# Performance work log

Measured on AMD Instinct MI355X. Metric: run time of the kernel, lower is better.

Reference implementation:

```python
import jax, jax.numpy as jnp
import numpy as np

B, FC, FRAMES, C = 8, 256, 512, 256


def conv1d(x, w, stride=1, pad=(0, 0), dil=1):
    # x: [N, Cin, L], w: [Cout, Cin, K]
    return jax.lax.conv_general_dilated(
        x, w, window_strides=(stride,), padding=[pad],
        rhs_dilation=(dil,), dimension_numbers=('NCH', 'OIH', 'NCH'))


def setup_inputs() -> dict:
    key = jax.random.key(0)
    ks = jax.random.split(key, 8)
    s = 0.05
    x = jax.random.normal(ks[0], (B, FC, FRAMES), dtype=jnp.float32)
    enc_w0 = jax.random.normal(ks[1], (128, 1, 7), dtype=jnp.float32) * s
    enc_w123 = jax.random.normal(ks[2], (3, 128, 128, 7), dtype=jnp.float32) * s
    enc_w4567 = jax.random.normal(ks[3], (4, 128, 128, 3), dtype=jnp.float32) * s
    enc_w8 = jax.random.normal(ks[4], (C, 128, 1), dtype=jnp.float32) * s
    main_w = jax.random.normal(ks[5], (8, C, C, 2), dtype=jnp.float32) * s
    gate_w = jax.random.normal(ks[6], (8, C, C, 2), dtype=jnp.float32) * s
    judge_w = jax.random.normal(ks[7], (1, C, 1), dtype=jnp.float32) * s
    return {'x': x, 'enc_w0': enc_w0, 'enc_w123': enc_w123,
            'enc_w4567': enc_w4567, 'enc_w8': enc_w8,
            'main_w': main_w, 'gate_w': gate_w, 'judge_w': judge_w}


def reference(x, enc_w0, enc_w123, enc_w4567, enc_w8, main_w, gate_w, judge_w):
    lrelu = lambda h: jax.nn.leaky_relu(h, 0.2)
    b = x.shape[0]
    # [B, FC, FRAMES] -> [B*FRAMES, 1, FC]: encode each frame's feature vector
    h = jnp.transpose(x, (0, 2, 1)).reshape(-1, 1, FC)
    h = lrelu(conv1d(h, enc_w0, stride=2, pad=(3, 3)))
    for i in range(3):
        h = lrelu(conv1d(h, enc_w123[i], stride=2, pad=(3, 3)))
    for i in range(4):
        h = lrelu(conv1d(h, enc_w4567[i], stride=2, pad=(1, 1)))
    h = conv1d(h, enc_w8)                       # [B*FRAMES, C, 1], no activation
    h = jnp.transpose(h.reshape(b, FRAMES, C), (0, 2, 1))  # [B, C, FRAMES]
    # WaveNet stack: causal pad + dilated k=2 convs + tanh*sigmoid gate + residual
    feats = jnp.zeros_like(h)
    for i in range(8):
        p = 2 ** i
        z = jnp.tanh(conv1d(h, main_w[i], pad=(p, 0), dil=p)) * \
            jax.nn.sigmoid(conv1d(h, gate_w[i], pad=(p, 0), dil=p))
        feats = feats + z
        h = z + h                              # channels always match -> residual
    latent = feats
    j = conv1d(latent, judge_w)[:, :, -1:]      # [B, 1, 1]
    return latent[:, :, -1:], j
```

## Files before the change

kernel.cpp:

```cpp
#include <hip/hip_runtime.h>
#include <math.h>

#define FC 256
#define NB 8
#define RS 136

typedef __attribute__((ext_vector_type(8))) _Float16 f16x8;
typedef __attribute__((ext_vector_type(4))) float f32x4;

__device__ __forceinline__ float lrelu(float v) { return fmaxf(v, 0.2f * v); }
__device__ __forceinline__ unsigned short f2h(float f) {
  _Float16 h = (_Float16)f;
  return *(unsigned short*)&h;
}
__device__ __forceinline__ void bar() { asm volatile("s_barrier" ::: "memory"); }
__device__ __forceinline__ void wait_lgkm0() { asm volatile("s_waitcnt lgkmcnt(0)" ::: "memory"); }

#define N1 344064
#define N2 196608
#define N3 32768
#define NTOT 573440
#define NWN 2097152

__global__ void pack_kernel(const float* __restrict__ w123,
                            const float* __restrict__ w4567,
                            const float* __restrict__ w8,
                            const float* __restrict__ mw,
                            const float* __restrict__ gw,
                            unsigned short* __restrict__ wp,
                            unsigned short* __restrict__ wn) {
  int idx = blockIdx.x * 512 + threadIdx.x;
  if (idx < N1) {
    int e = idx & 7, lane = (idx >> 3) & 63, ct = (idx >> 9) & 7, ks = (idx >> 12) & 3, t = idx >> 14;
    int l = t / 7, kw = t % 7;
    int co = ct * 16 + (lane & 15), ci = ks * 32 + (lane >> 4) * 8 + e;
    wp[idx] = f2h(w123[(((l * 128 + co) * 128) + ci) * 7 + kw]);
  } else if (idx < N1 + N2) {
    int k = idx - N1;
    int e = k & 7, lane = (k >> 3) & 63, ct = (k >> 9) & 7, ks = (k >> 12) & 3, t = k >> 14;
    int l = t / 3, kw = t % 3;
    int co = ct * 16 + (lane & 15), ci = ks * 32 + (lane >> 4) * 8 + e;
    wp[idx] = f2h(w4567[(((l * 128 + co) * 128) + ci) * 3 + kw]);
  } else if (idx < NTOT) {
    int k = idx - N1 - N2;
    int e = k & 7, lane = (k >> 3) & 63, ct = (k >> 9) & 15, ks = (k >> 13) & 3;
    int co = ct * 16 + (lane & 15), ci = ks * 32 + (lane >> 4) * 8 + e;
    wp[idx] = f2h(w8[co * 128 + ci]);
  } else if (idx < NTOT + NWN) {
    int k2 = idx - NTOT;
    int li = k2 >> 18, w = k2 & 262143;
    int e = w & 7, lane = (w >> 3) & 63, rt = (w >> 9) & 31, k32 = w >> 14;
    int row = rt * 16 + (lane & 15), k = k32 * 32 + (lane >> 4) * 8 + e;
    int ch = row >> 1, mat = row & 1, kw = k >> 8, ci = k & 255;
    const float* src = mat ? gw : mw;
    wn[k2] = f2h(src[(((size_t)li * 256 + ch) * 256 + ci) * 2 + kw]);
  }
}

template<int KW, int POFF, int PIN, int POUT, int MC, int MN, int OM>
__device__ __forceinline__ void mlayer_d2(const unsigned short* __restrict__ wp,
                                          const unsigned short* __restrict__ sin0,
                                          const unsigned short* __restrict__ sin1,
                                          unsigned short* __restrict__ sout0,
                                          unsigned short* __restrict__ sout1,
                                          unsigned short* __restrict__ gact,
                                          int tid, int frame0) {
  constexpr int HRIN = PIN / 2 + 4;
  constexpr int HROUT = POUT / 2 + 4;
  constexpr int Nt = (POUT + 15) / 16;
  constexpr int MNg = Nt / MN;
  constexpr int MCg = 8 / MNg;
  static_assert(MC * MCg == 8, "cout tiling must cover 128 channels");
  constexpr int NS = KW * 4;
  constexpr int DA = NS < 6 ? NS : 6;
  constexpr int DB = NS < 3 ? NS : 3;

  const int wid = tid >> 6, lane = tid & 63, nl = lane & 15, q = lane >> 4;
  const int q8 = q * 8;
  const int mcg = wid / MNg, mng = wid % MNg;
  const int ct0 = mcg * MC, nt0 = mng * MN;

  const unsigned short* sins[2] = {sin0, sin1};
  unsigned short* souts[2] = {sout0, sout1};

  int jj[MN]; bool val[MN]; int rb[MN][KW]; int rx[MN][KW];
#pragma unroll
  for (int jn = 0; jn < MN; ++jn) {
    int n = (nt0 + jn) * 16 + nl;
    val[jn] = (n < POUT);
    jj[jn] = val[jn] ? n : 0;
#pragma unroll
    for (int kw = 0; kw < KW; ++kw) {
      int P = 2 * jj[jn] + kw - POFF + 4;
      int row = (P & 1) * HRIN + (P >> 1);
      rb[jn][kw] = row * 128;
      rx[jn][kw] = (row & 7) << 3;
    }
  }
  const unsigned short* wl = wp + (size_t)ct0 * 512 + lane * 8;

  f32x4 acc[MC][MN][2];
#pragma unroll
  for (int i = 0; i < MC; ++i)
#pragma unroll
    for (int jn = 0; jn < MN; ++jn)
#pragma unroll
      for (int f = 0; f < 2; ++f) acc[i][jn][f] = (f32x4){0.f, 0.f, 0.f, 0.f};

  f16x8 A[DA][MC], B[DB][MN][2];
#pragma unroll
  for (int s = 0; s < DA; ++s)
#pragma unroll
    for (int i = 0; i < MC; ++i)
      A[s][i] = *(const f16x8*)(wl + (size_t)s * 4096 + i * 512);
#pragma unroll
  for (int s = 0; s < DB; ++s) {
    const int kw = s >> 2, ks = s & 3;
#pragma unroll
    for (int jn = 0; jn < MN; ++jn)
#pragma unroll
      for (int f = 0; f < 2; ++f)
        B[s][jn][f] = *(const f16x8*)(sins[f] + rb[jn][kw] + ((ks * 32 + q8) ^ rx[jn][kw]));
  }
#pragma unroll
  for (int s = 0; s < NS; ++s) {
    const int sa = s % DA, sb = s % DB;
#pragma unroll
    for (int i = 0; i < MC; ++i)
#pragma unroll
      for (int jn = 0; jn < MN; ++jn)
#pragma unroll
        for (int f = 0; f < 2; ++f)
          acc[i][jn][f] = __builtin_amdgcn_mfma_f32_16x16x32_f16(A[sa][i], B[sb][jn][f], acc[i][jn][f], 0, 0, 0);
    if (s + DA < NS) {
#pragma unroll
      for (int i = 0; i < MC; ++i)
        A[sa][i] = *(const f16x8*)(wl + (size_t)(s + DA) * 4096 + i * 512);
    }
    if (s + DB < NS) {
      const int kw = (s + DB) >> 2, ks = (s + DB) & 3;
#pragma unroll
      for (int jn = 0; jn < MN; ++jn)
#pragma unroll
        for (int f = 0; f < 2; ++f)
          B[sb][jn][f] = *(const f16x8*)(sins[f] + rb[jn][kw] + ((ks * 32 + q8) ^ rx[jn][kw]));
    }
  }

#pragma unroll
  for (int f = 0; f < 2; ++f) {
#pragma unroll
    for (int i = 0; i < MC; ++i) {
#pragma unroll
      for (int jn = 0; jn < MN; ++jn) {
        if (!val[jn]) continue;
        unsigned int lo = (unsigned)f2h(lrelu(acc[i][jn][f][0])) | ((unsigned)f2h(lrelu(acc[i][jn][f][1])) << 16);
        unsigned int hi = (unsigned)f2h(lrelu(acc[i][jn][f][2])) | ((unsigned)f2h(lrelu(acc[i][jn][f][3])) << 16);
        const int j = jj[jn];
        if (OM == 1) {
          *(uint2*)(gact + ((size_t)(frame0 + f) * POUT + j) * 128 + (ct0 + i) * 16 + q * 4) = make_uint2(lo, hi);
        } else {
          const int row = (j & 1) * HROUT + (j >> 1) + 2;
          const int off = row * 128 + (((ct0 + i) * 16 + (q >> 1) * 8) ^ ((row & 7) << 3)) + (q & 1) * 4;
          *(uint2*)(souts[f] + off) = make_uint2(lo, hi);
        }
      }
    }
  }
  if (OM == 0) {
    constexpr int DEND = ((POUT - 1) >> 1) + 3;
    constexpr int NZ = 2 + (HROUT - DEND);
#pragma unroll
    for (int f = 0; f < 2; ++f) {
      unsigned int* zp = (unsigned int*)souts[f];
      for (int s2 = tid; s2 < 2 * NZ * 64; s2 += 512) {
        int col = s2 & 63, rr = s2 >> 6;
        int par = rr / NZ, rz = rr % NZ;
        int row = rz < 2 ? rz : DEND + rz - 2;
        zp[((par * HROUT + row) << 6) + col] = 0;
      }
    }
    __syncthreads();
  }
}

__global__ __launch_bounds__(512, 2)
void encoder1(const float* __restrict__ x, const float* __restrict__ w0,
              const unsigned short* __restrict__ wp123,
              const unsigned short* __restrict__ wp4,
              unsigned short* __restrict__ act4g) {
  __shared__ __align__(16) unsigned short actA[34816];
  __shared__ __align__(16) unsigned short actB[18432];
  const int tid = threadIdx.x;
  const int frame0 = blockIdx.x * 2;
  const int bb = frame0 >> 8;
  const int t0 = (frame0 & 255) + 256;

  float* s_x0 = (float*)actB;
  float* s_x1 = (float*)actB + 272;

  if (tid < 256) s_x0[3 + tid] = x[((bb << 8) + tid) * 512 + t0];
  else           s_x1[3 + (tid & 255)] = x[((bb << 8) + (tid & 255)) * 512 + t0 + 1];
  if (tid < 3)                 { s_x0[tid] = 0.f; s_x1[tid] = 0.f; }
  if (tid >= 259 && tid < 262) { s_x0[tid] = 0.f; s_x1[tid] = 0.f; }
  wait_lgkm0();
  bar();

  {
    const int c = tid & 127;
    const int sel = tid >> 7;
    const int cblk = c & 120, clo = c & 7;
    float wv[7];
#pragma unroll
    for (int k = 0; k < 7; ++k) wv[k] = w0[c * 7 + k];
#pragma unroll
    for (int f = 0; f < 2; ++f) {
      const float* sx = f ? s_x1 : s_x0;
      unsigned short* aA = actA + f * 17408;
      for (int j = sel * 32; j < sel * 32 + 32; ++j) {
        float s = 0.f;
#pragma unroll
        for (int k = 0; k < 7; ++k) s += wv[k] * sx[2 * j + k];
        int row = ((j & 1) ? 68 : 0) + (j >> 1) + 2;
        aA[row * 128 + (cblk ^ ((row & 7) << 3)) + clo] = f2h(lrelu(s));
      }
    }
#pragma unroll
    for (int f = 0; f < 2; ++f) {
      unsigned int* zp = (unsigned int*)(actA + f * 17408);
      for (int s2 = tid; s2 < 2 * 4 * 64; s2 += 512) {
        int col = s2 & 63;
        int rr = s2 >> 6;
        int par = rr >> 2, r2 = rr & 3;
        int row = (r2 < 2) ? r2 : (64 + r2);
        zp[((par * 68 + row) << 6) + col] = 0;
      }
    }
  }
  wait_lgkm0();
  bar();

  mlayer_d2<7, 3, 128, 64, 2, 2, 0>(wp123,         actA, actA + 17408, actB, actB + 9216,
                                    nullptr, tid, frame0);
  mlayer_d2<7, 3, 64, 32, 1, 2, 0>(wp123 + 114688, actB, actB + 9216, actA, actA + 17408,
                                    nullptr, tid, frame0);
  mlayer_d2<7, 3, 32, 16, 1, 1, 0>(wp123 + 229376, actA, actA + 17408,
                                    actA + 5120, actA + 17408 + 5120, nullptr, tid, frame0);
  mlayer_d2<3, 1, 16, 8, 1, 1, 1>(wp4,             actA + 5120, actA + 17408 + 5120,
                                    nullptr, nullptr, act4g, tid, frame0);
}

template<int KW, int POFF, int PIN, int POUT, int FPB, int COUT, int MC, int MN, int OM, bool FLATIN>
__device__ __forceinline__ void mlayer(const unsigned short* __restrict__ wp,
                                       const unsigned short* __restrict__ sin_,
                                       unsigned short* __restrict__ sout,
                                       float* __restrict__ gout,
                                       int tid, int frame0) {
  constexpr int HRIN  = PIN / 2 + 4;
  constexpr int HROUT = POUT / 2 + 4;
  constexpr int NVAL = POUT * FPB;
  constexpr int Nt = (NVAL + 15) / 16;
  constexpr int Ct = COUT / 16;
  constexpr int MCg = Ct / MC, MNg = Nt / MN;
  constexpr int KS = 4;
  constexpr int NS = KW * KS;
  constexpr int DA = NS < 6 ? NS : 6;
  constexpr int DB = NS < 3 ? NS : 3;
  constexpr int L2P = POUT == 1 ? 0 : POUT == 2 ? 1 : POUT == 4 ? 2 : POUT == 8 ? 3 :
                      POUT == 16 ? 4 : POUT == 32 ? 5 : 6;

  const int wid = tid >> 6, lane = tid & 63, nl = lane & 15, q = lane >> 4;

  for (int mac = wid; mac < MCg * MNg; mac += 8) {
    const int mcg = mac / MNg, mng = mac % MNg;
    const int ct0 = mcg * MC, nt0 = mng * MN;
    int jj[MN]; bool val[MN];
#pragma unroll
    for (int jn = 0; jn < MN; ++jn) {
      int n = (nt0 + jn) * 16 + nl;
      val[jn] = (n < NVAL);
      jj[jn] = val[jn] ? n : 0;
    }
    int rofs[MN][KW];
#pragma unroll
    for (int jn = 0; jn < MN; ++jn) {
      const int f = jj[jn] >> L2P, j = jj[jn] & (POUT - 1);
#pragma unroll
      for (int kw = 0; kw < KW; ++kw) {
        if (FLATIN) {
          rofs[jn][kw] = jj[jn] * RS + q * 8;
        } else {
          int P = 2 * j + kw - POFF + 4;
          rofs[jn][kw] = (f * 2 * HRIN + (P & 1) * HRIN + (P >> 1)) * RS + q * 8;
        }
      }
    }
    int abase[MC];
#pragma unroll
    for (int i = 0; i < MC; ++i) abase[i] = (ct0 + i) * 512 + lane * 8;

    f32x4 acc[MC][MN];
#pragma unroll
    for (int i = 0; i < MC; ++i)
#pragma unroll
      for (int jn = 0; jn < MN; ++jn) acc[i][jn] = (f32x4){0.f, 0.f, 0.f, 0.f};

    f16x8 A[DA][MC], B[DB][MN];
#pragma unroll
    for (int s = 0; s < DA; ++s) {
      const int kw = s / KS, ks = s % KS;
#pragma unroll
      for (int i = 0; i < MC; ++i)
        A[s][i] = *(const f16x8*)(wp + (size_t)(kw * KS + ks) * (Ct * 512) + abase[i]);
    }
#pragma unroll
    for (int s = 0; s < DB; ++s) {
      const int kw = s / KS, ks = s % KS;
#pragma unroll
      for (int jn = 0; jn < MN; ++jn)
        B[s][jn] = *(const f16x8*)(sin_ + rofs[jn][kw] + ks * 32);
    }
#pragma unroll
    for (int s = 0; s < NS; ++s) {
      const int sa = s % DA, sb = s % DB;
#pragma unroll
      for (int i = 0; i < MC; ++i)
#pragma unroll
        for (int jn = 0; jn < MN; ++jn)
          acc[i][jn] = __builtin_amdgcn_mfma_f32_16x16x32_f16(A[sa][i], B[sb][jn], acc[i][jn], 0, 0, 0);
      if (s + DA < NS) {
        const int kw = (s + DA) / KS, ks = (s + DA) % KS;
#pragma unroll
        for (int i = 0; i < MC; ++i)
          A[sa][i] = *(const f16x8*)(wp + (size_t)(kw * KS + ks) * (Ct * 512) + abase[i]);
      }
      if (s + DB < NS) {
        const int kw = (s + DB) / KS, ks = (s + DB) % KS;
#pragma unroll
        for (int jn = 0; jn < MN; ++jn)
          B[sb][jn] = *(const f16x8*)(sin_ + rofs[jn][kw] + ks * 32);
      }
    }
#pragma unroll
    for (int i = 0; i < MC; ++i) {
#pragma unroll
      for (int jn = 0; jn < MN; ++jn) {
        if (OM == 3) {
          if (val[jn]) {
            const int frame = frame0 + jj[jn];
            float4 v = make_float4(acc[i][jn][0], acc[i][jn][1], acc[i][jn][2], acc[i][jn][3]);
            *(float4*)(gout + (size_t)frame * 256 + (ct0 + i) * 16 + q * 4) = v;
          }
        } else if (OM == 2) {
          if (val[jn]) {
            unsigned int lo = (unsigned)f2h(lrelu(acc[i][jn][0])) | ((unsigned)f2h(lrelu(acc[i][jn][1])) << 16);
            unsigned int hi = (unsigned)f2h(lrelu(acc[i][jn][2])) | ((unsigned)f2h(lrelu(acc[i][jn][3])) << 16);
            *(uint2*)(sout + (size_t)jj[jn] * RS + (ct0 + i) * 16 + q * 4) = make_uint2(lo, hi);
          }
        } else {
          if (val[jn]) {
            const int f = jj[jn] >> L2P, j = jj[jn] & (POUT - 1);
            const int row = f * 2 * HROUT + (j & 1) * HROUT + (j >> 1) + 2;
            unsigned int lo = (unsigned)f2h(lrelu(acc[i][jn][0])) | ((unsigned)f2h(lrelu(acc[i][jn][1])) << 16);
            unsigned int hi = (unsigned)f2h(lrelu(acc[i][jn][2])) | ((unsigned)f2h(lrelu(acc[i][jn][3])) << 16);
            *(uint2*)(sout + (size_t)row * RS + (ct0 + i) * 16 + q * 4) = make_uint2(lo, hi);
          }
        }
      }
    }
  }
  if (OM == 0) {
    constexpr int DEND = ((POUT - 1) >> 1) + 3;
    constexpr int NZ = 2 + (HROUT - DEND);
    constexpr int TOTU = FPB * 2 * NZ * (RS / 2);
    unsigned int* zp = (unsigned int*)sout;
    for (int s2 = tid; s2 < TOTU; s2 += 512) {
      int col = s2 % 68;
      int rr = s2 / 68;
      int fr = rr / (2 * NZ), r2 = rr % (2 * NZ);
      int par = r2 / NZ, rz = r2 % NZ;
      int row = rz < 2 ? rz : DEND + rz - 2;
      zp[((size_t)(fr * 2 + par) * HROUT + row) * 68 + col] = 0;
    }
    __syncthreads();
  } else if (OM == 2) {
    __syncthreads();
  }
}

__global__ __launch_bounds__(512)
void encoder2(const unsigned short* __restrict__ act4g,
              const unsigned short* __restrict__ wp4,
              const unsigned short* __restrict__ wp8,
              float* __restrict__ h) {
  __shared__ __align__(16) unsigned short actP[17408];
  __shared__ __align__(16) unsigned short actQ[13056];
  __shared__ __align__(16) unsigned short actR[2176];
  const int tid = threadIdx.x;
  const int frame0 = blockIdx.x * 8;

  {
    uint4 z4 = make_uint4(0, 0, 0, 0);
    for (int s = tid; s < 2176; s += 512) ((uint4*)actP)[s] = z4;
    for (int s = tid; s < 1632; s += 512) ((uint4*)actQ)[s] = z4;
    for (int s = tid; s < 272; s += 512) ((uint4*)actR)[s] = z4;
  }
  __syncthreads();
  for (int c = tid; c < 1024; c += 512) {
    int f = c >> 7, rem = c & 127, pos = rem >> 4, o = (rem & 15) * 8;
    uint4 v = *(const uint4*)(act4g + ((size_t)(frame0 + f) * 8 + pos) * 128 + o);
    int P = pos + 4;
    int row = (P & 1) * 8 + (P >> 1);
    *(uint4*)(actP + ((size_t)f * 16 + row) * RS + o) = v;
  }
  __syncthreads();

  mlayer<3, 1, 8, 4, 8, 128, 2, 1, 0, false>(wp4 + 49152,  actP, actQ, nullptr, tid, frame0);
  mlayer<3, 1, 4, 2, 8, 128, 1, 1, 0, false>(wp4 + 98304,  actQ, actP, nullptr, tid, frame0);
  mlayer<3, 1, 2, 1, 8, 128, 1, 1, 2, false>(wp4 + 147456, actP, actR, nullptr, tid, frame0);
  mlayer<1, 0, 1, 1, 8, 256, 1, 1, 3, true>(wp8,           actR, nullptr, h, tid, frame0);
}

__global__ __launch_bounds__(256)
void wnet_kernel(const unsigned short* __restrict__ wn,
                 const float* __restrict__ hsrc, float* __restrict__ hdst,
                 float* __restrict__ feats, const float* __restrict__ jw,
                 float* __restrict__ out, int li) {
  const int npos = 128 >> li, p = 1 << li, N = npos * 8, lnp = 7 - li;
  const int tid = threadIdx.x;
  const int nb = blockIdx.x >> 2, mb = blockIdx.x & 3;
  const int n0 = nb * 16;
  __shared__ __align__(16) unsigned short sB[16 * 520];
  __shared__ float jls[8];

  for (int c = tid; c < 1024; c += 256) {
    const int nr = c >> 6, o = (c & 63) * 8;
    const int n = n0 + nr;
    unsigned short tmp[8] = {0, 0, 0, 0, 0, 0, 0, 0};
    if (n < N) {
      const int b = n >> lnp, kk = n & (npos - 1);
      const int t = 255 - (kk << (li + 1));
      const float* src = (o < 256) ? hsrc + ((size_t)(b * 256 + t - p)) * 256 + o
                                   : hsrc + ((size_t)(b * 256 + t)) * 256 + (o - 256);
      float4 v0 = *(const float4*)(src);
      float4 v1 = *(const float4*)(src + 4);
      tmp[0] = f2h(v0.x); tmp[1] = f2h(v0.y); tmp[2] = f2h(v0.z); tmp[3] = f2h(v0.w);
      tmp[4] = f2h(v1.x); tmp[5] = f2h(v1.y); tmp[6] = f2h(v1.z); tmp[7] = f2h(v1.w);
    }
    unsigned int u0 = (unsigned)tmp[0] | ((unsigned)tmp[1] << 16);
    unsigned int u1 = (unsigned)tmp[2] | ((unsigned)tmp[3] << 16);
    unsigned int u2 = (unsigned)tmp[4] | ((unsigned)tmp[5] << 16);
    unsigned int u3 = (unsigned)tmp[6] | ((unsigned)tmp[7] << 16);
    *(uint4*)(sB + (size_t)nr * 520 + o) = make_uint4(u0, u1, u2, u3);
  }
  __syncthreads();

  const int wid = tid >> 6, lane = tid & 63, nl = lane & 15, q = lane >> 4;
  f32x4 acc[2];
  acc[0] = (f32x4){0.f, 0.f, 0.f, 0.f};
  acc[1] = (f32x4){0.f, 0.f, 0.f, 0.f};
  int arow[2];
#pragma unroll
  for (int i = 0; i < 2; ++i) arow[i] = (mb * 8 + wid * 2 + i) * 512 + lane * 8;
  const int bofs = nl * 520 + q * 8;

  f16x8 A[4][2], Bv[2];
#pragma unroll
  for (int s = 0; s < 4; ++s)
#pragma unroll
    for (int i = 0; i < 2; ++i) A[s][i] = *(const f16x8*)(wn + arow[i] + (size_t)s * 16384);
#pragma unroll
  for (int s = 0; s < 2; ++s) Bv[s] = *(const f16x8*)(sB + bofs + s * 32);
#pragma unroll
  for (int s = 0; s < 16; ++s) {
    const int sa = s & 3, sb = s & 1;
    acc[0] = __builtin_amdgcn_mfma_f32_16x16x32_f16(A[sa][0], Bv[sb], acc[0], 0, 0, 0);
    acc[1] = __builtin_amdgcn_mfma_f32_16x16x32_f16(A[sa][1], Bv[sb], acc[1], 0, 0, 0);
    if (s + 4 < 16) {
#pragma unroll
      for (int i = 0; i < 2; ++i) A[sa][i] = *(const f16x8*)(wn + arow[i] + (size_t)(s + 4) * 16384);
    }
    if (s + 2 < 16) Bv[sb] = *(const f16x8*)(sB + bofs + (s + 2) * 32);
  }

  const int n = n0 + nl;
  if (li < 7) {
    if (n < N) {
      const int b = n >> lnp, kk = n & (npos - 1);
      const int t = 255 - (kk << (li + 1));
      const size_t rowoff = ((size_t)(b * 256 + t)) * 256;
#pragma unroll
      for (int i = 0; i < 2; ++i) {
        const int ch = mb * 64 + (wid * 2 + i) * 8 + q * 2;
        const float z0 = tanhf(acc[i][0]) * (1.f / (1.f + expf(-acc[i][1])));
        const float z1 = tanhf(acc[i][2]) * (1.f / (1.f + expf(-acc[i][3])));
        float2 hv = *(const float2*)(hsrc + rowoff + ch);
        *(float2*)(hdst + rowoff + ch) = make_float2(hv.x + z0, hv.y + z1);
        if (kk == 0) {
          float* fp = feats + b * 256 + ch;
          if (li == 0) { fp[0] = z0; fp[1] = z1; }
          else         { fp[0] += z0; fp[1] += z1; }
        }
      }
    }
  } else {
    if (tid < 8) jls[tid] = 0.f;
    __syncthreads();
    if (n < N) {
      const int b = n;
      float partial = 0.f;
#pragma unroll
      for (int i = 0; i < 2; ++i) {
        const int ch = mb * 64 + (wid * 2 + i) * 8 + q * 2;
        const float z0 = tanhf(acc[i][0]) * (1.f / (1.f + expf(-acc[i][1])));
        const float z1 = tanhf(acc[i][2]) * (1.f / (1.f + expf(-acc[i][3])));
        const float* fp = feats + b * 256 + ch;
        const float f0 = fp[0] + z0;
        const float f1 = fp[1] + z1;
        *(float2*)(out + b * 256 + ch) = make_float2(f0, f1);
        partial += f0 * jw[ch] + f1 * jw[ch + 1];
      }
      atomicAdd(&jls[b], partial);
    }
    __syncthreads();
    if (tid < 8) atomicAdd(out + NB * 256 + tid, jls[tid]);
  }
}

extern "C" void kernel_launch(void* const* d_in, const int* in_sizes, int n_in,
                              void* d_out, int out_size, void* d_ws, size_t ws_size,
                              hipStream_t stream) {
  const float* x     = (const float*)d_in[0];
  const float* w0    = (const float*)d_in[1];
  const float* w123  = (const float*)d_in[2];
  const float* w4567 = (const float*)d_in[3];
  const float* w8    = (const float*)d_in[4];
  const float* mw    = (const float*)d_in[5];
  const float* gw    = (const float*)d_in[6];
  const float* jw    = (const float*)d_in[7];
  float* out = (float*)d_out;

  float* ws = (float*)d_ws;
  unsigned short* act4g = (unsigned short*)ws;
  float* h0    = ws + 1048576;
  float* h1    = ws + 1572864;
  float* feats = ws + 2097152;
  unsigned short* wp = (unsigned short*)(ws + 2099200);
  unsigned short* wn = (unsigned short*)(ws + 2385920);

  hipMemsetAsync(out + NB * 256, 0, NB * sizeof(float), stream);
  pack_kernel<<<5216, 512, 0, stream>>>(w123, w4567, w8, mw, gw, wp, wn);
  encoder1<<<1024, 512, 0, stream>>>(x, w0, wp, wp + N1, act4g);
  encoder2<<<256, 512, 0, stream>>>(act4g, wp + N1, wp + N1 + N2, h0);

  float* hs = h0; float* hd = h1;
  for (int i = 0; i < 8; ++i) {
    const unsigned short* wl = wn + (size_t)i * 262144;
    const int N = (128 >> i) * 8;
    const int nN = (N + 15) / 16;
    wnet_kernel<<<4 * nN, 256, 0, stream>>>(wl, hs, hd, feats, jw, out, i);
    float* tmp = hd; hd = hs; hs = tmp;
  }
}
```

Before: 207.7 us.

## Fuse WaveNet layers 2-7 and judge reduction into one per-batch kernel

```diff
diff --git a/kernel.cpp b/kernel.cpp
--- a/kernel.cpp
+++ b/kernel.cpp
@@ -424,14 +424,12 @@
 __global__ __launch_bounds__(256)
 void wnet_kernel(const unsigned short* __restrict__ wn,
                  const float* __restrict__ hsrc, float* __restrict__ hdst,
-                 float* __restrict__ feats, const float* __restrict__ jw,
-                 float* __restrict__ out, int li) {
+                 float* __restrict__ feats, int li) {
   const int npos = 128 >> li, p = 1 << li, N = npos * 8, lnp = 7 - li;
   const int tid = threadIdx.x;
   const int nb = blockIdx.x >> 2, mb = blockIdx.x & 3;
   const int n0 = nb * 16;
   __shared__ __align__(16) unsigned short sB[16 * 520];
-  __shared__ float jls[8];
 
   for (int c = tid; c < 1024; c += 256) {
     const int nr = c >> 6, o = (c & 63) * 8;
@@ -484,47 +482,127 @@
   }
 
   const int n = n0 + nl;
-  if (li < 7) {
-    if (n < N) {
-      const int b = n >> lnp, kk = n & (npos - 1);
+  if (n < N) {
+    const int b = n >> lnp, kk = n & (npos - 1);
+    const int t = 255 - (kk << (li + 1));
+    const size_t rowoff = ((size_t)(b * 256 + t)) * 256;
+#pragma unroll
+    for (int i = 0; i < 2; ++i) {
+      const int ch = mb * 64 + (wid * 2 + i) * 8 + q * 2;
+      const float z0 = tanhf(acc[i][0]) * (1.f / (1.f + expf(-acc[i][1])));
+      const float z1 = tanhf(acc[i][2]) * (1.f / (1.f + expf(-acc[i][3])));
+      float2 hv = *(const float2*)(hsrc + rowoff + ch);
+      *(float2*)(hdst + rowoff + ch) = make_float2(hv.x + z0, hv.y + z1);
+      if (kk == 0) {
+        float* fp = feats + b * 256 + ch;
+        if (li == 0) { fp[0] = z0; fp[1] = z1; }
+        else { fp[0] += z0; fp[1] += z1; }
+      }
+    }
+  }
+}
+
+__global__ __launch_bounds__(1024)
+void wnet_fused(const unsigned short* __restrict__ wn,
+                float* __restrict__ h0, float* __restrict__ h1,
+                const float* __restrict__ feats, const float* __restrict__ jw,
+                float* __restrict__ out) {
+  const int b = blockIdx.x;
+  const int tid = threadIdx.x;
+  const int wid = tid >> 6, lane = tid & 63, nl = lane & 15, q = lane >> 4;
+  __shared__ __align__(16) unsigned short sB[32 * 520];
+  __shared__ float sfeats[256];
+  __shared__ float red[256];
+
+  if (tid < 256) sfeats[tid] = feats[b * 256 + tid];
+  float* hs = h0; float* hd = h1;
+
+  for (int li = 2; li < 8; ++li) {
+    const int p = 1 << li, npos = 128 >> li;
+    const int Pt = (npos + 15) >> 4;
+    const unsigned short* wl = wn + (size_t)li * 262144;
+    __syncthreads();
+
+    for (int c = tid; c < npos * 64; c += 1024) {
+      const int kk = c >> 6, o = (c & 63) * 8;
       const int t = 255 - (kk << (li + 1));
-      const size_t rowoff = ((size_t)(b * 256 + t)) * 256;
-#pragma unroll
-      for (int i = 0; i < 2; ++i) {
-        const int ch = mb * 64 + (wid * 2 + i) * 8 + q * 2;
-        const float z0 = tanhf(acc[i][0]) * (1.f / (1.f + expf(-acc[i][1])));
-        const float z1 = tanhf(acc[i][2]) * (1.f / (1.f + expf(-acc[i][3])));
-        float2 hv = *(const float2*)(hsrc + rowoff + ch);
-        *(float2*)(hdst + rowoff + ch) = make_float2(hv.x + z0, hv.y + z1);
-        if (kk == 0) {
-          float* fp = feats + b * 256 + ch;
-          if (li == 0) { fp[0] = z0; fp[1] = z1; }
-          else         { fp[0] += z0; fp[1] += z1; }
+      const float* src = (o < 256) ? hs + ((size_t)(b * 256 + t - p)) * 256 + o
+                                   : hs + ((size_t)(b * 256 + t)) * 256 + (o - 256);
+      float4 v0 = *(const float4*)(src);
+      float4 v1 = *(const float4*)(src + 4);
+      unsigned short tmp[8];
+      tmp[0] = f2h(v0.x); tmp[1] = f2h(v0.y); tmp[2] = f2h(v0.z); tmp[3] = f2h(v0.w);
+      tmp[4] = f2h(v1.x); tmp[5] = f2h(v1.y); tmp[6] = f2h(v1.z); tmp[7] = f2h(v1.w);
+      unsigned int u0 = (unsigned)tmp[0] | ((unsigned)tmp[1] << 16);
+      unsigned int u1 = (unsigned)tmp[2] | ((unsigned)tmp[3] << 16);
+      unsigned int u2 = (unsigned)tmp[4] | ((unsigned)tmp[5] << 16);
+      unsigned int u3 = (unsigned)tmp[6] | ((unsigned)tmp[7] << 16);
+      *(uint4*)(sB + (size_t)kk * 520 + o) = make_uint4(u0, u1, u2, u3);
+    }
+    __syncthreads();
+
+    for (int task = wid; task < 16 * Pt; task += 16) {
+      const int rp = task & 15, pt = task >> 4;
+      f32x4 acc[2];
+      acc[0] = (f32x4){0.f, 0.f, 0.f, 0.f};
+      acc[1] = (f32x4){0.f, 0.f, 0.f, 0.f};
+      int arow[2];
+#pragma unroll
+      for (int i = 0; i < 2; ++i) arow[i] = (rp * 2 + i) * 512 + lane * 8;
+      const int bofs = (pt * 16 + nl) * 520 + q * 8;
+
+      f16x8 A[4][2], Bv[2];
+#pragma unroll
+      for (int s = 0; s < 4; ++s)
+#pragma unroll
+        for (int i = 0; i < 2; ++i) A[s][i] = *(const f16x8*)(wl + arow[i] + (size_t)s * 16384);
+#pragma unroll
+      for (int s = 0; s < 2; ++s) Bv[s] = *(const f16x8*)(sB + bofs + s * 32);
+#pragma unroll
+      for (int s = 0; s < 16; ++s) {
+        const int sa = s & 3, sb = s & 1;
+        acc[0] = __builtin_amdgcn_mfma_f32_16x16x32_f16(A[sa][0], Bv[sb], acc[0], 0, 0, 0);
+        acc[1] = __builtin_amdgcn_mfma_f32_16x16x32_f16(A[sa][1], Bv[sb], acc[1], 0, 0, 0);
+        if (s + 4 < 16) {
+#pragma unroll
+          for (int i = 0; i < 2; ++i) A[sa][i] = *(const f16x8*)(wl + arow[i] + (size_t)(s + 4) * 16384);
         }
-      }
-    }
-  } else {
-    if (tid < 8) jls[tid] = 0.f;
+        if (s + 2 < 16) Bv[sb] = *(const f16x8*)(sB + bofs + (s + 2) * 32);
+      }
+
+      const int kk = pt * 16 + nl;
+      if (kk < npos) {
+        const int t = 255 - (kk << (li + 1));
+        const size_t rowoff = ((size_t)(b * 256 + t)) * 256;
+#pragma unroll
+        for (int i = 0; i < 2; ++i) {
+          const int ch = (rp * 2 + i) * 8 + q * 2;
+          const float z0 = tanhf(acc[i][0]) * (1.f / (1.f + expf(-acc[i][1])));
+          const float z1 = tanhf(acc[i][2]) * (1.f / (1.f + expf(-acc[i][3])));
+          float2 hv = *(const float2*)(hs + rowoff + ch);
+          *(float2*)(hd + rowoff + ch) = make_float2(hv.x + z0, hv.y + z1);
+          if (kk == 0) {
+            sfeats[ch]     += z0;
+            sfeats[ch + 1] += z1;
+          }
+        }
+      }
+    }
+    float* tsw = hs; hs = hd; hd = tsw;
+  }
+
+  __syncthreads();
+  if (tid < 256) {
+    const float v = sfeats[tid];
+    out[b * 256 + tid] = v;
+    red[tid] = v * jw[tid];
+  }
+  __syncthreads();
+  for (int s = 128; s > 0; s >>= 1) {
+    if (tid < s) red[tid] += red[tid + s];
     __syncthreads();
-    if (n < N) {
-      const int b = n;
-      float partial = 0.f;
-#pragma unroll
-      for (int i = 0; i < 2; ++i) {
-        const int ch = mb * 64 + (wid * 2 + i) * 8 + q * 2;
-        const float z0 = tanhf(acc[i][0]) * (1.f / (1.f + expf(-acc[i][1])));
-        const float z1 = tanhf(acc[i][2]) * (1.f / (1.f + expf(-acc[i][3])));
-        const float* fp = feats + b * 256 + ch;
-        const float f0 = fp[0] + z0;
-        const float f1 = fp[1] + z1;
-        *(float2*)(out + b * 256 + ch) = make_float2(f0, f1);
-        partial += f0 * jw[ch] + f1 * jw[ch + 1];
-      }
-      atomicAdd(&jls[b], partial);
-    }
-    __syncthreads();
-    if (tid < 8) atomicAdd(out + NB * 256 + tid, jls[tid]);
-  }
+  }
+  if (tid == 0) out[NB * 256 + b] = red[0];
 }
 
 extern "C" void kernel_launch(void* const* d_in, const int* in_sizes, int n_in,
@@ -548,17 +626,11 @@
   unsigned short* wp = (unsigned short*)(ws + 2099200);
   unsigned short* wn = (unsigned short*)(ws + 2385920);
 
-  hipMemsetAsync(out + NB * 256, 0, NB * sizeof(float), stream);
   pack_kernel<<<5216, 512, 0, stream>>>(w123, w4567, w8, mw, gw, wp, wn);
   encoder1<<<1024, 512, 0, stream>>>(x, w0, wp, wp + N1, act4g);
   encoder2<<<256, 512, 0, stream>>>(act4g, wp + N1, wp + N1 + N2, h0);
 
-  float* hs = h0; float* hd = h1;
-  for (int i = 0; i < 8; ++i) {
-    const unsigned short* wl = wn + (size_t)i * 262144;
-    const int N = (128 >> i) * 8;
-    const int nN = (N + 15) / 16;
-    wnet_kernel<<<4 * nN, 256, 0, stream>>>(wl, hs, hd, feats, jw, out, i);
-    float* tmp = hd; hd = hs; hs = tmp;
-  }
-}
+  wnet_kernel<<<4 * 64, 256, 0, stream>>>(wn,          h0, h1, feats, 0);
+  wnet_kernel<<<4 * 32, 256, 0, stream>>>(wn + 262144, h1, h0, feats, 1);
+  wnet_fused<<<NB, 1024, 0, stream>>>(wn, h0, h1, feats, jw, out);
+}
```

New measurement: 272.6 us. +31.3%, slower.
